# Kernel optimization log

Measured on AMD Instinct MI355X. Metric: run time of the kernel, lower is better.

The kernel has to match this reference:

```python
import jax, jax.numpy as jnp
import numpy as np

T, D, H, E, K = 8192, 2048, 7168, 8, 2


def setup_inputs() -> dict:
    key = jax.random.key(0)
    ks = jax.random.split(key, 5)
    s = 0.02
    return {
        "x": jax.random.normal(ks[0], (T, D), jnp.float32),
        "gate_w": jax.random.normal(ks[1], (E, D), jnp.float32) * s,
        "w1": jax.random.normal(ks[2], (E, H, D), jnp.float32) * s,
        "w2": jax.random.normal(ks[3], (E, H, D), jnp.float32) * s,
        "w3": jax.random.normal(ks[4], (E, H, D), jnp.float32) * s,
    }


def reference(x, gate_w, w1, w2, w3):
    # gate logits [T, E]
    logits = x @ gate_w.T
    vals, idx = jax.lax.top_k(logits, K)                      # [T, K]
    w = jax.nn.softmax(vals.astype(jnp.float32), axis=-1).astype(x.dtype)
    # per-token routing weight for each expert (0 if not selected) [T, E]
    tok = jnp.arange(x.shape[0])
    expert_w = jnp.zeros((x.shape[0], E), x.dtype).at[tok[:, None], idx].add(w)

    # scan over experts: dense SwiGLU per expert, weighted accumulate
    def body(acc, ws):
        w1e, w2e, w3e, we = ws  # [H,D],[H,D],[H,D],[T]
        y = (jax.nn.silu(x @ w1e.T) * (x @ w3e.T)) @ w2e      # [T, D]
        return acc + we[:, None] * y, None

    res, _ = jax.lax.scan(body, jnp.zeros_like(x), (w1, w2, w3, expert_w.T))
    return res
```

## Files before the change

### kernel.cpp

```cpp
#include <hip/hip_runtime.h>

#define TT   8192
#define DDIM 2048
#define HDIM 7168
#define NEXP 8
#define MT   32
#define NT1  (HDIM / 128)
#define NT2  (DDIM / 256)

typedef __attribute__((ext_vector_type(8))) short bf16x8;
typedef __attribute__((ext_vector_type(4))) short short4v;
typedef __attribute__((ext_vector_type(4))) float f32x4;

__device__ __forceinline__ unsigned short f2bf(float f) {
  unsigned int u = __builtin_bit_cast(unsigned int, f);
  u += 0x7fffu + ((u >> 16) & 1u);
  return (unsigned short)(u >> 16);
}

__device__ __forceinline__ void gload_lds16(const void* gp, void* lp) {
  __builtin_amdgcn_global_load_lds((__attribute__((address_space(1))) void*)gp,
                                   (__attribute__((address_space(3))) void*)lp,
                                   16, 0, 0);
}

__device__ __forceinline__ void mfma16(f32x4& c, bf16x8 a, bf16x8 b) {
  c = __builtin_amdgcn_mfma_f32_16x16x32_bf16(a, b, c, 0, 0, 0);
}

__device__ __forceinline__ void wg_barrier() {
  asm volatile("" ::: "memory");
  __builtin_amdgcn_s_barrier();
  asm volatile("" ::: "memory");
}

#define PH(H, BA, BB, RDB, STG, SRCP, SOFF, VM)                              \
  do {                                                                       \
    if (RDB) {                                                               \
      _Pragma("unroll")                                                      \
      for (int n = 0; n < 4; ++n)                                            \
        bfr[n] = *(const bf16x8*)(smem + (BB) + rB + n * 1024);              \
    }                                                                        \
    _Pragma("unroll")                                                        \
    for (int m = 0; m < 4; ++m)                                              \
      af[m] = *(const bf16x8*)(smem + (BA) + rA + ((H) + m) * 1024);         \
    if ((STG) >= 0) {                                                        \
      gload_lds16(SRCP[0] + (SOFF), smem + (STG) + wid * 2048);              \
      gload_lds16(SRCP[1] + (SOFF), smem + (STG) + wid * 2048 + 1024);       \
    }                                                                        \
    wg_barrier();                                                            \
    asm volatile("s_waitcnt lgkmcnt(0)" ::: "memory");                       \
    __builtin_amdgcn_sched_barrier(0);                                       \
    __builtin_amdgcn_s_setprio(1);                                           \
    _Pragma("unroll")                                                        \
    for (int n = 0; n < 4; ++n) {                                            \
      _Pragma("unroll")                                                      \
      for (int m = 0; m < 4; ++m)                                            \
        mfma16(acc[(H) + m][n], af[m], bfr[n]);                              \
    }                                                                        \
    __builtin_amdgcn_s_setprio(0);                                           \
    if ((VM) == 6) asm volatile("s_waitcnt vmcnt(6)" ::: "memory");          \
    if ((VM) == 0) asm volatile("s_waitcnt vmcnt(0)" ::: "memory");          \
    wg_barrier();                                                            \
  } while (0)

#define ITER_FULL(kb)                                                        \
  PH(0, 0,     32768,  1, 81920,  asrc, (kb) + 192, -1);                     \
  PH(4, 0,     32768,  0, 32768,  bsrc, (kb) + 256, -1);                     \
  PH(0, 16384, 49152,  1, 0,      asrc, (kb) + 256, -1);                     \
  PH(4, 16384, 49152,  0, 49152,  bsrc, (kb) + 320,  6);                     \
  PH(0, 65536, 98304,  1, 16384,  asrc, (kb) + 320, -1);                     \
  PH(4, 65536, 98304,  0, 98304,  bsrc, (kb) + 384, -1);                     \
  PH(0, 81920, 114688, 1, 65536,  asrc, (kb) + 384, -1);                     \
  PH(4, 81920, 114688, 0, 114688, bsrc, (kb) + 448,  6);

#define ITER_LAST(kb)                                                        \
  PH(0, 0,     32768,  1, 81920,  asrc, (kb) + 192, -1);                     \
  PH(4, 0,     32768,  0, -1,     asrc, 0,          -1);                     \
  PH(0, 16384, 49152,  1, -1,     asrc, 0,          -1);                     \
  PH(4, 16384, 49152,  0, -1,     asrc, 0,           0);                     \
  PH(0, 65536, 98304,  1, -1,     asrc, 0,          -1);                     \
  PH(4, 65536, 98304,  0, -1,     asrc, 0,          -1);                     \
  PH(0, 81920, 114688, 1, -1,     asrc, 0,          -1);                     \
  PH(4, 81920, 114688, 0, -1,     asrc, 0,          -1);

#define PROLOGUE()                                                           \
  do {                                                                       \
    gload_lds16(asrc[0] + 0,   smem + 0      + wid * 2048);                  \
    gload_lds16(asrc[1] + 0,   smem + 0      + wid * 2048 + 1024);           \
    gload_lds16(bsrc[0] + 0,   smem + 32768  + wid * 2048);                  \
    gload_lds16(bsrc[1] + 0,   smem + 32768  + wid * 2048 + 1024);           \
    gload_lds16(asrc[0] + 64,  smem + 16384  + wid * 2048);                  \
    gload_lds16(asrc[1] + 64,  smem + 16384  + wid * 2048 + 1024);           \
    gload_lds16(bsrc[0] + 64,  smem + 49152  + wid * 2048);                  \
    gload_lds16(bsrc[1] + 64,  smem + 49152  + wid * 2048 + 1024);           \
    gload_lds16(bsrc[0] + 128, smem + 98304  + wid * 2048);                  \
    gload_lds16(bsrc[1] + 128, smem + 98304  + wid * 2048 + 1024);           \
    gload_lds16(asrc[0] + 128, smem + 65536  + wid * 2048);                  \
    gload_lds16(asrc[1] + 128, smem + 65536  + wid * 2048 + 1024);           \
    gload_lds16(bsrc[0] + 192, smem + 114688 + wid * 2048);                  \
    gload_lds16(bsrc[1] + 192, smem + 114688 + wid * 2048 + 1024);           \
    asm volatile("s_waitcnt vmcnt(6)" ::: "memory");                         \
    wg_barrier();                                                            \
  } while (0)

__global__ __launch_bounds__(256) void cvt_bf16_kernel(const float* __restrict__ src,
                                                       unsigned short* __restrict__ dst,
                                                       long n4) {
  long i = (long)blockIdx.x * 256 + threadIdx.x;
  long stride = (long)gridDim.x * 256;
  for (; i < n4; i += stride) {
    float4 v = ((const float4*)src)[i];
    short4v s;
    s[0] = (short)f2bf(v.x); s[1] = (short)f2bf(v.y);
    s[2] = (short)f2bf(v.z); s[3] = (short)f2bf(v.w);
    ((short4v*)dst)[i] = s;
  }
}

__global__ __launch_bounds__(256) void gate_kernel(const float* __restrict__ x,
                                                   const float* __restrict__ gw,
                                                   int* __restrict__ route_e,
                                                   float* __restrict__ route_w,
                                                   int* __restrict__ counts) {
  int t = blockIdx.x;
  int tid = threadIdx.x;
  const float* xr = x + (size_t)t * DDIM;
  float p[NEXP];
#pragma unroll
  for (int e = 0; e < NEXP; ++e) p[e] = 0.f;
#pragma unroll
  for (int c = 0; c < DDIM / (256 * 4); ++c) {
    int d = (c * 256 + tid) * 4;
    float4 xv = *(const float4*)(xr + d);
#pragma unroll
    for (int e = 0; e < NEXP; ++e) {
      float4 wv = *(const float4*)(gw + (size_t)e * DDIM + d);
      p[e] += xv.x * wv.x + xv.y * wv.y + xv.z * wv.z + xv.w * wv.w;
    }
  }
  __shared__ float red[NEXP][4];
  int lane = tid & 63, wid = tid >> 6;
#pragma unroll
  for (int e = 0; e < NEXP; ++e) {
    float v = p[e];
    for (int o = 32; o > 0; o >>= 1) v += __shfl_down(v, o);
    if (lane == 0) red[e][wid] = v;
  }
  __syncthreads();
  if (tid == 0) {
    float lg[NEXP];
#pragma unroll
    for (int e = 0; e < NEXP; ++e) lg[e] = red[e][0] + red[e][1] + red[e][2] + red[e][3];
    int i0 = 0;
#pragma unroll
    for (int e = 1; e < NEXP; ++e) if (lg[e] > lg[i0]) i0 = e;
    int i1 = -1;
#pragma unroll
    for (int e = 0; e < NEXP; ++e) {
      if (e == i0) continue;
      if (i1 < 0 || lg[e] > lg[i1]) i1 = e;
    }
    float w0 = 1.f / (1.f + __expf(lg[i1] - lg[i0]));
    float w1 = 1.f - w0;
    route_e[t * 2 + 0] = i0;  route_e[t * 2 + 1] = i1;
    route_w[t * 2 + 0] = w0;  route_w[t * 2 + 1] = w1;
    atomicAdd(&counts[i0], 1);
    atomicAdd(&counts[i1], 1);
  }
}

__global__ void scan_kernel(const int* __restrict__ counts, int* __restrict__ offsets,
                            int* __restrict__ cursor) {
  if (threadIdx.x == 0 && blockIdx.x == 0) {
    int o = 0;
    for (int e = 0; e < NEXP; ++e) { offsets[e] = o; cursor[e] = o; o += counts[e]; }
  }
}

__global__ __launch_bounds__(256) void scatter_kernel(const int* __restrict__ route_e,
                                                      const float* __restrict__ route_w,
                                                      int* __restrict__ cursor,
                                                      int* __restrict__ tok_list,
                                                      float* __restrict__ tok_w) {
  int t = blockIdx.x * 256 + threadIdx.x;
  if (t >= TT) return;
#pragma unroll
  for (int s = 0; s < 2; ++s) {
    int e = route_e[t * 2 + s];
    int p = atomicAdd(&cursor[e], 1);
    tok_list[p] = t;
    tok_w[p] = route_w[t * 2 + s];
  }
}

__global__ __launch_bounds__(256) void transpose_w2_kernel(const float* __restrict__ w2,
                                                           unsigned short* __restrict__ w2t,
                                                           int expert_fixed) {
  int e = expert_fixed >= 0 ? expert_fixed : (int)blockIdx.z;
  const float* src = w2 + (size_t)e * HDIM * DDIM;
  unsigned short* dst = w2t + (expert_fixed >= 0 ? (size_t)0 : (size_t)e * DDIM * HDIM);
  int h0 = blockIdx.x * 64, d0 = blockIdx.y * 64;
  __shared__ __align__(8) unsigned short tile[64 * 66];
  int tid = threadIdx.x;
  int hr = tid >> 2;
#pragma unroll
  for (int j = 0; j < 4; ++j) {
    int f4 = (tid & 3) + j * 4;
    float4 v = *(const float4*)(src + (size_t)(h0 + hr) * DDIM + d0 + f4 * 4);
    unsigned int lo = (unsigned int)f2bf(v.x) | ((unsigned int)f2bf(v.y) << 16);
    unsigned int hi = (unsigned int)f2bf(v.z) | ((unsigned int)f2bf(v.w) << 16);
    char* bp = (char*)tile + hr * 132 + f4 * 8;
    *(unsigned int*)bp = lo;
    *(unsigned int*)(bp + 4) = hi;
  }
  __syncthreads();
  int dr = tid >> 2;
  int hbase = (tid & 3) * 16;
  unsigned short vals[16];
#pragma unroll
  for (int i = 0; i < 16; ++i)
    vals[i] = *(unsigned short*)((char*)tile + (hbase + i) * 132 + dr * 2);
  unsigned short* op = dst + (size_t)(d0 + dr) * HDIM + h0 + hbase;
#pragma unroll
  for (int j = 0; j < 4; ++j) {
    short4v s;
    s[0] = (short)vals[j * 4 + 0]; s[1] = (short)vals[j * 4 + 1];
    s[2] = (short)vals[j * 4 + 2]; s[3] = (short)vals[j * 4 + 3];
    *(short4v*)(op + j * 4) = s;
  }
}

__global__ __launch_bounds__(512, 2) void gemm1_kernel(
    const unsigned short* __restrict__ xbf, const unsigned short* __restrict__ w1b,
    const unsigned short* __restrict__ w3b, const int* __restrict__ tok_list,
    const int* __restrict__ counts, const int* __restrict__ offsets,
    unsigned short* __restrict__ g, int expert_fixed) {
  __shared__ __align__(16) char smem[133120];
  constexpr int NI = DDIM / 128;

  int nwg = gridDim.x;
  int orig = blockIdx.x;
  int wg = (orig & 7) * (nwg >> 3) + (orig >> 3);
  int mt = wg & (MT - 1);
  int rem = wg >> 5;
  int nt = rem % NT1;
  int e = expert_fixed >= 0 ? expert_fixed : rem / NT1;

  int cnt = counts[e];
  int mbase = mt * 256;
  if (mbase >= cnt) return;
  int off = offsets[e];
  int gshift = expert_fixed >= 0 ? 0 : off;
  int rows = cnt - mbase; if (rows > 256) rows = 256;

  const unsigned short* w1e = expert_fixed >= 0 ? w1b : w1b + (size_t)e * HDIM * DDIM;
  const unsigned short* w3e = expert_fixed >= 0 ? w3b : w3b + (size_t)e * HDIM * DDIM;

  int tid = threadIdx.x, lane = tid & 63, wid = tid >> 6;
  int wr = wid >> 2, wc = wid & 3;

  int r16 = lane >> 2;
  int csrc = (lane & 3) ^ ((lane >> 3) & 3);
  const char* asrc[2]; const char* bsrc[2];
#pragma unroll
  for (int j = 0; j < 2; ++j) {
    int r = wid * 32 + j * 16 + r16;
    int m = mbase + r; if (m > cnt - 1) m = cnt - 1;
    int tok = tok_list[off + m];
    asrc[j] = (const char*)xbf + (size_t)tok * (DDIM * 2) + csrc * 16;
    const char* base = (r < 128)
        ? (const char*)w1e + (size_t)(nt * 128 + r) * (DDIM * 2)
        : (const char*)w3e + (size_t)(nt * 128 + r - 128) * (DDIM * 2);
    bsrc[j] = base + csrc * 16;
  }
  int rA = (wr * 128 + (lane & 15)) * 64 + (((lane >> 4) ^ ((lane >> 1) & 3)) * 16);
  int rB = (wc * 64  + (lane & 15)) * 64 + (((lane >> 4) ^ ((lane >> 1) & 3)) * 16);

  f32x4 zv = {0.f, 0.f, 0.f, 0.f};
  f32x4 acc[8][4];
#pragma unroll
  for (int m = 0; m < 8; ++m)
#pragma unroll
    for (int n = 0; n < 4; ++n) acc[m][n] = zv;
  bf16x8 af[4], bfr[4];

  PROLOGUE();
#pragma unroll 1
  for (int i = 0; i < NI - 1; ++i) {
    size_t kb = (size_t)i * 256;
    ITER_FULL(kb);
  }
  {
    size_t kb = (size_t)(NI - 1) * 256;
    ITER_LAST(kb);
  }

  float* hb = (float*)smem;
  if (wc < 2) {
#pragma unroll
    for (int m = 0; m < 8; ++m)
#pragma unroll
      for (int q = 0; q < 4; ++q) {
        int row = wr * 128 + m * 16 + (lane >> 4) * 4 + q;
        int col = wc * 64 + (lane & 15);
#pragma unroll
        for (int n = 0; n < 4; ++n)
          hb[row * 130 + col + n * 16] = acc[m][n][q];
      }
  }
  asm volatile("s_waitcnt lgkmcnt(0)" ::: "memory");
  wg_barrier();
  if (wc >= 2) {
#pragma unroll
    for (int m = 0; m < 8; ++m)
#pragma unroll
      for (int q = 0; q < 4; ++q) {
        int row = wr * 128 + m * 16 + (lane >> 4) * 4 + q;
        if (row >= rows) continue;
        size_t grow = (size_t)(mbase + row + gshift);
        int colbase = (wc - 2) * 64 + (lane & 15);
        unsigned short* gp = g + grow * HDIM + nt * 128 + colbase;
#pragma unroll
        for (int n = 0; n < 4; ++n) {
          float h1 = hb[row * 130 + colbase + n * 16];
          float h3 = acc[m][n][q];
          float gv = (h1 / (1.f + __expf(-h1))) * h3;
          gp[n * 16] = f2bf(gv);
        }
      }
  }
}

__global__ __launch_bounds__(512, 2) void gemm2_kernel(
    const unsigned short* __restrict__ g, const unsigned short* __restrict__ w2t,
    const int* __restrict__ tok_list, const float* __restrict__ tok_w,
    const int* __restrict__ counts, const int* __restrict__ offsets,
    float* __restrict__ out, int expert_fixed) {
  __shared__ __align__(16) char smem[131072];
  constexpr int NI = HDIM / 128;

  int nwg = gridDim.x;
  int orig = blockIdx.x;
  int wg = (orig & 7) * (nwg >> 3) + (orig >> 3);
  int mt = wg & (MT - 1);
  int rem = wg >> 5;
  int nt = rem % NT2;
  int e = expert_fixed >= 0 ? expert_fixed : rem / NT2;

  int cnt = counts[e];
  int mbase = mt * 256;
  if (mbase >= cnt) return;
  int off = offsets[e];
  int gshift = expert_fixed >= 0 ? 0 : off;
  int nbase = nt * 256;
  int rows = cnt - mbase; if (rows > 256) rows = 256;
  const unsigned short* w2te = w2t + (expert_fixed >= 0 ? (size_t)0 : (size_t)e * DDIM * HDIM);

  int tid = threadIdx.x, lane = tid & 63, wid = tid >> 6;
  int wr = wid >> 2, wc = wid & 3;

  int r16 = lane >> 2;
  int csrc = (lane & 3) ^ ((lane >> 3) & 3);
  const char* asrc[2]; const char* bsrc[2];
#pragma unroll
  for (int j = 0; j < 2; ++j) {
    int r = wid * 32 + j * 16 + r16;
    int m = mbase + r; if (m > cnt - 1) m = cnt - 1;
    asrc[j] = (const char*)g + (size_t)(m + gshift) * (HDIM * 2) + csrc * 16;
    bsrc[j] = (const char*)w2te + (size_t)(nbase + r) * (HDIM * 2) + csrc * 16;
  }
  int rA = (wr * 128 + (lane & 15)) * 64 + (((lane >> 4) ^ ((lane >> 1) & 3)) * 16);
  int rB = (wc * 64  + (lane & 15)) * 64 + (((lane >> 4) ^ ((lane >> 1) & 3)) * 16);

  f32x4 zv = {0.f, 0.f, 0.f, 0.f};
  f32x4 acc[8][4];
#pragma unroll
  for (int m = 0; m < 8; ++m)
#pragma unroll
    for (int n = 0; n < 4; ++n) acc[m][n] = zv;
  bf16x8 af[4], bfr[4];

  PROLOGUE();
#pragma unroll 1
  for (int i = 0; i < NI - 1; ++i) {
    size_t kb = (size_t)i * 256;
    ITER_FULL(kb);
  }
  {
    size_t kb = (size_t)(NI - 1) * 256;
    ITER_LAST(kb);
  }

#pragma unroll
  for (int m = 0; m < 8; ++m)
#pragma unroll
    for (int q = 0; q < 4; ++q) {
      int row = wr * 128 + m * 16 + (lane >> 4) * 4 + q;
      if (row >= rows) continue;
      int mi = mbase + row;
      int tok = tok_list[off + mi];
      float wt = tok_w[off + mi];
      float* op = out + (size_t)tok * DDIM + nbase + wc * 64 + (lane & 15);
#pragma unroll
      for (int n = 0; n < 4; ++n)
        atomicAdd(op + n * 16, acc[m][n][q] * wt);
    }
}

extern "C" void kernel_launch(void* const* d_in, const int* in_sizes, int n_in,
                              void* d_out, int out_size, void* d_ws, size_t ws_size,
                              hipStream_t stream) {
  const float* x      = (const float*)d_in[0];
  const float* gate_w = (const float*)d_in[1];
  const float* w1     = (const float*)d_in[2];
  const float* w2     = (const float*)d_in[3];
  const float* w3     = (const float*)d_in[4];
  float* out = (float*)d_out;
  char* ws = (char*)d_ws;

  size_t o = 0;
  int* counts  = (int*)(ws + o);
  int* offsets = counts + 8;
  int* cursor  = counts + 16;
  o += 256;
  int*   route_e = (int*)(ws + o);   o += (size_t)TT * 2 * 4;
  float* route_w = (float*)(ws + o); o += (size_t)TT * 2 * 4;
  int*   tok_list = (int*)(ws + o);  o += (size_t)TT * 2 * 4;
  float* tok_w = (float*)(ws + o);   o += (size_t)TT * 2 * 4;
  unsigned short* xbf = (unsigned short*)(ws + o); o += (size_t)TT * DDIM * 2;
  size_t fixed = o;

  const size_t WSZ = (size_t)HDIM * DDIM;
  const size_t wbf_full = (size_t)NEXP * WSZ * 2;
  const size_t gfull = (size_t)TT * 2 * HDIM * 2;

  hipMemsetAsync(counts, 0, 8 * sizeof(int), stream);
  hipMemsetAsync(out, 0, (size_t)TT * DDIM * sizeof(float), stream);
  cvt_bf16_kernel<<<4096, 256, 0, stream>>>(x, xbf, (long)TT * DDIM / 4);
  gate_kernel<<<TT, 256, 0, stream>>>(x, gate_w, route_e, route_w, counts);
  scan_kernel<<<1, 64, 0, stream>>>(counts, offsets, cursor);
  scatter_kernel<<<(TT + 255) / 256, 256, 0, stream>>>(route_e, route_w, cursor, tok_list, tok_w);

  if (ws_size >= fixed + 3 * wbf_full + gfull) {
    unsigned short* w1b = (unsigned short*)(ws + fixed);
    unsigned short* w3b = w1b + NEXP * WSZ;
    unsigned short* w2t = w3b + NEXP * WSZ;
    unsigned short* gbuf = w2t + NEXP * WSZ;
    cvt_bf16_kernel<<<8192, 256, 0, stream>>>(w1, w1b, (long)(NEXP * WSZ / 4));
    cvt_bf16_kernel<<<8192, 256, 0, stream>>>(w3, w3b, (long)(NEXP * WSZ / 4));
    transpose_w2_kernel<<<dim3(HDIM / 64, DDIM / 64, NEXP), 256, 0, stream>>>(w2, w2t, -1);
    gemm1_kernel<<<MT * NT1 * NEXP, 512, 0, stream>>>(
        xbf, w1b, w3b, tok_list, counts, offsets, gbuf, -1);
    gemm2_kernel<<<MT * NT2 * NEXP, 512, 0, stream>>>(
        gbuf, w2t, tok_list, tok_w, counts, offsets, out, -1);
  } else {
    unsigned short* w1b = (unsigned short*)(ws + fixed);
    unsigned short* w3b = w1b + WSZ;
    unsigned short* w2t = w3b + WSZ;
    unsigned short* gbuf = w2t + WSZ;
    for (int e = 0; e < NEXP; ++e) {
      cvt_bf16_kernel<<<4096, 256, 0, stream>>>(w1 + (size_t)e * WSZ, w1b, (long)(WSZ / 4));
      cvt_bf16_kernel<<<4096, 256, 0, stream>>>(w3 + (size_t)e * WSZ, w3b, (long)(WSZ / 4));
      transpose_w2_kernel<<<dim3(HDIM / 64, DDIM / 64, 1), 256, 0, stream>>>(w2, w2t, e);
      gemm1_kernel<<<MT * NT1, 512, 0, stream>>>(
          xbf, w1b, w3b, tok_list, counts, offsets, gbuf, e);
      gemm2_kernel<<<MT * NT2, 512, 0, stream>>>(
          gbuf, w2t, tok_list, tok_w, counts, offsets, out, e);
    }
  }
}
```

Measured before the change: 2.491 ms.

## Double-buffer LDS fragment reads to overlap ds_read with MFMA in GEMM phases

Each phase now issues the LDS reads for the next phase's A/B fragments into alternate register buffers (af0/af1, bf0/bf1) before running the current phase's MFMAs. The lgkmcnt waits are partial, so only the data needed now must have arrived. The reads use inline-asm ds_read_b128, and the vmcnt waits are retuned. The aim is to hide LDS read latency behind matrix math, at the cost of more vector registers, which could affect occupancy or cause spills.

```diff
diff --git a/kernel.cpp b/kernel.cpp
--- a/kernel.cpp
+++ b/kernel.cpp
@@ -11,6 +11,7 @@
 typedef __attribute__((ext_vector_type(8))) short bf16x8;
 typedef __attribute__((ext_vector_type(4))) short short4v;
 typedef __attribute__((ext_vector_type(4))) float f32x4;
+typedef const __attribute__((address_space(3))) char* lds_ptr;
 
 __device__ __forceinline__ unsigned short f2bf(float f) {
   unsigned int u = __builtin_bit_cast(unsigned int, f);
@@ -28,61 +29,72 @@
   c = __builtin_amdgcn_mfma_f32_16x16x32_bf16(a, b, c, 0, 0, 0);
 }
 
+__device__ __forceinline__ bf16x8 ds_read128(lds_ptr p) {
+  bf16x8 r;
+  asm volatile("ds_read_b128 %0, %1" : "=&v"(r) : "v"(p));
+  return r;
+}
+
 __device__ __forceinline__ void wg_barrier() {
   asm volatile("" ::: "memory");
   __builtin_amdgcn_s_barrier();
   asm volatile("" ::: "memory");
 }
 
-#define PH(H, BA, BB, RDB, STG, SRCP, SOFF, VM)                              \
+#define PH2(HH, AF, BF, NBA, AFN, NBB, BFN, STG, SRCP, SOFF, LGK, VM)        \
   do {                                                                       \
-    if (RDB) {                                                               \
+    if ((NBA) >= 0) {                                                        \
+      _Pragma("unroll")                                                      \
+      for (int m = 0; m < 4; ++m)                                            \
+        AFN[m] = ds_read128(lds3 + (NBA) + rA + m * 1024);                   \
+    }                                                                        \
+    if ((NBB) >= 0) {                                                        \
       _Pragma("unroll")                                                      \
       for (int n = 0; n < 4; ++n)                                            \
-        bfr[n] = *(const bf16x8*)(smem + (BB) + rB + n * 1024);              \
+        BFN[n] = ds_read128(lds3 + (NBB) + rB + n * 1024);                   \
     }                                                                        \
-    _Pragma("unroll")                                                        \
-    for (int m = 0; m < 4; ++m)                                              \
-      af[m] = *(const bf16x8*)(smem + (BA) + rA + ((H) + m) * 1024);         \
     if ((STG) >= 0) {                                                        \
       gload_lds16(SRCP[0] + (SOFF), smem + (STG) + wid * 2048);              \
       gload_lds16(SRCP[1] + (SOFF), smem + (STG) + wid * 2048 + 1024);       \
     }                                                                        \
     wg_barrier();                                                            \
-    asm volatile("s_waitcnt lgkmcnt(0)" ::: "memory");                       \
+    if ((LGK) == 8) asm volatile("s_waitcnt lgkmcnt(8)" ::: "memory");       \
+    if ((LGK) == 4) asm volatile("s_waitcnt lgkmcnt(4)" ::: "memory");       \
+    if ((LGK) == 0) asm volatile("s_waitcnt lgkmcnt(0)" ::: "memory");       \
     __builtin_amdgcn_sched_barrier(0);                                       \
     __builtin_amdgcn_s_setprio(1);                                           \
     _Pragma("unroll")                                                        \
     for (int n = 0; n < 4; ++n) {                                            \
       _Pragma("unroll")                                                      \
       for (int m = 0; m < 4; ++m)                                            \
-        mfma16(acc[(H) + m][n], af[m], bfr[n]);                              \
+        mfma16(acc[(HH) + m][n], AF[m], BF[n]);                              \
     }                                                                        \
     __builtin_amdgcn_s_setprio(0);                                           \
-    if ((VM) == 6) asm volatile("s_waitcnt vmcnt(6)" ::: "memory");          \
+    __builtin_amdgcn_sched_barrier(0);                                       \
+    if ((VM) == 8) asm volatile("s_waitcnt vmcnt(8)" ::: "memory");          \
     if ((VM) == 0) asm volatile("s_waitcnt vmcnt(0)" ::: "memory");          \
     wg_barrier();                                                            \
   } while (0)
 
-#define ITER_FULL(kb)                                                        \
-  PH(0, 0,     32768,  1, 81920,  asrc, (kb) + 192, -1);                     \
-  PH(4, 0,     32768,  0, 32768,  bsrc, (kb) + 256, -1);                     \
-  PH(0, 16384, 49152,  1, 0,      asrc, (kb) + 256, -1);                     \
-  PH(4, 16384, 49152,  0, 49152,  bsrc, (kb) + 320,  6);                     \
-  PH(0, 65536, 98304,  1, 16384,  asrc, (kb) + 320, -1);                     \
-  PH(4, 65536, 98304,  0, 98304,  bsrc, (kb) + 384, -1);                     \
-  PH(0, 81920, 114688, 1, 65536,  asrc, (kb) + 384, -1);                     \
-  PH(4, 81920, 114688, 0, 114688, bsrc, (kb) + 448,  6);
-
-#define ITER_LAST(kb)                                                        \
-  PH(0, 0,     32768,  1, 81920,  asrc, (kb) + 192, -1);                     \
-  PH(4, 0,     32768,  0, -1,     asrc, 0,          -1);                     \
-  PH(0, 16384, 49152,  1, -1,     asrc, 0,          -1);                     \
-  PH(4, 16384, 49152,  0, -1,     asrc, 0,           0);                     \
-  PH(0, 65536, 98304,  1, -1,     asrc, 0,          -1);                     \
-  PH(4, 65536, 98304,  0, -1,     asrc, 0,          -1);                     \
-  PH(0, 81920, 114688, 1, -1,     asrc, 0,          -1);                     \
-  PH(4, 81920, 114688, 0, -1,     asrc, 0,          -1);
+#define ITER_FULL2(kb)                                                         \
+  PH2(0, af1, bf0, 4096,  af0, -1,     bf1, 81920,  asrc, (kb) + 192, 4, 8);   \
+  PH2(4, af0, bf0, 16384, af1, 49152,  bf1, 32768,  bsrc, (kb) + 256, 8, 8);   \
+  PH2(0, af1, bf1, 20480, af0, -1,     bf0, 0,      asrc, (kb) + 256, 4, 8);   \
+  PH2(4, af0, bf1, 65536, af1, 98304,  bf0, 49152,  bsrc, (kb) + 320, 8, 8);   \
+  PH2(0, af1, bf0, 69632, af0, -1,     bf1, 16384,  asrc, (kb) + 320, 4, 8);   \
+  PH2(4, af0, bf0, 81920, af1, 114688, bf1, 98304,  bsrc, (kb) + 384, 8, 8);   \
+  PH2(0, af1, bf1, 86016, af0, -1,     bf0, 65536,  asrc, (kb) + 384, 4, 8);   \
+  PH2(4, af0, bf1, 0,     af1, 32768,  bf0, 114688, bsrc, (kb) + 448, 8, 8);
+
+#define ITER_LAST2(kb)                                                         \
+  PH2(0, af1, bf0, 4096,  af0, -1,     bf1, 81920, asrc, (kb) + 192, 4, 8);    \
+  PH2(4, af0, bf0, 16384, af1, 49152,  bf1, -1,    asrc, 0,          8, 8);    \
+  PH2(0, af1, bf1, 20480, af0, -1,     bf0, -1,    asrc, 0,          4, 8);    \
+  PH2(4, af0, bf1, 65536, af1, 98304,  bf0, -1,    asrc, 0,          8, 0);    \
+  PH2(0, af1, bf0, 69632, af0, -1,     bf1, -1,    asrc, 0,          4, 8);    \
+  PH2(4, af0, bf0, 81920, af1, 114688, bf1, -1,    asrc, 0,          8, 8);    \
+  PH2(0, af1, bf1, 86016, af0, -1,     bf0, -1,    asrc, 0,          4, 8);    \
+  PH2(4, af0, bf1, -1,    af1, -1,     bf0, -1,    asrc, 0,          0, 8);
 
 #define PROLOGUE()                                                           \
   do {                                                                       \
@@ -102,6 +114,12 @@
     gload_lds16(bsrc[1] + 192, smem + 114688 + wid * 2048 + 1024);           \
     asm volatile("s_waitcnt vmcnt(6)" ::: "memory");                         \
     wg_barrier();                                                            \
+    _Pragma("unroll")                                                        \
+    for (int m = 0; m < 4; ++m)                                              \
+      af1[m] = ds_read128(lds3 + 0 + rA + m * 1024);                         \
+    _Pragma("unroll")                                                        \
+    for (int n = 0; n < 4; ++n)                                              \
+      bf0[n] = ds_read128(lds3 + 32768 + rB + n * 1024);                     \
   } while (0)
 
 __global__ __launch_bounds__(256) void cvt_bf16_kernel(const float* __restrict__ src,
@@ -259,6 +277,7 @@
 
   int tid = threadIdx.x, lane = tid & 63, wid = tid >> 6;
   int wr = wid >> 2, wc = wid & 3;
+  lds_ptr lds3 = (lds_ptr)smem;
 
   int r16 = lane >> 2;
   int csrc = (lane & 3) ^ ((lane >> 3) & 3);
@@ -283,17 +302,17 @@
   for (int m = 0; m < 8; ++m)
 #pragma unroll
     for (int n = 0; n < 4; ++n) acc[m][n] = zv;
-  bf16x8 af[4], bfr[4];
+  bf16x8 af0[4], af1[4], bf0[4], bf1[4];
 
   PROLOGUE();
 #pragma unroll 1
   for (int i = 0; i < NI - 1; ++i) {
     size_t kb = (size_t)i * 256;
-    ITER_FULL(kb);
+    ITER_FULL2(kb);
   }
   {
     size_t kb = (size_t)(NI - 1) * 256;
-    ITER_LAST(kb);
+    ITER_LAST2(kb);
   }
 
   float* hb = (float*)smem;
@@ -359,6 +378,7 @@
 
   int tid = threadIdx.x, lane = tid & 63, wid = tid >> 6;
   int wr = wid >> 2, wc = wid & 3;
+  lds_ptr lds3 = (lds_ptr)smem;
 
   int r16 = lane >> 2;
   int csrc = (lane & 3) ^ ((lane >> 3) & 3);
@@ -379,17 +399,17 @@
   for (int m = 0; m < 8; ++m)
 #pragma unroll
     for (int n = 0; n < 4; ++n) acc[m][n] = zv;
-  bf16x8 af[4], bfr[4];
+  bf16x8 af0[4], af1[4], bf0[4], bf1[4];
 
   PROLOGUE();
 #pragma unroll 1
   for (int i = 0; i < NI - 1; ++i) {
     size_t kb = (size_t)i * 256;
-    ITER_FULL(kb);
+    ITER_FULL2(kb);
   }
   {
     size_t kb = (size_t)(NI - 1) * 256;
-    ITER_LAST(kb);
+    ITER_LAST2(kb);
   }
 
 #pragma unroll
```

Result: slower. 3.156 ms (+26.7%).

## Merge half-phases into full 8x4 MFMA phases with joint A/B staging

Applied to the files above, without the earlier changes.

Restructures the software-pipelined GEMM main loop from eight half-tile phases per iteration into four full phases. Each phase now loads all 8 A fragments and 4 B fragments, issues 32 MFMAs, and stages both the A and B tiles for a later k-block at once. The prologue and vmcnt waits are adjusted to match. This halves the number of workgroup barriers per iteration and gives larger MFMA bursts, at the cost of more live VGPRs for fragments and a shallower prefetch lead for the B tiles.

```diff
diff --git a/kernel.cpp b/kernel.cpp
--- a/kernel.cpp
+++ b/kernel.cpp
@@ -34,19 +34,21 @@
   asm volatile("" ::: "memory");
 }
 
-#define PH(H, BA, BB, RDB, STG, SRCP, SOFF, VM)                              \
+#define PH4(BA, BB, SA, AO, SB, BO, VM)                                      \
   do {                                                                       \
-    if (RDB) {                                                               \
-      _Pragma("unroll")                                                      \
-      for (int n = 0; n < 4; ++n)                                            \
-        bfr[n] = *(const bf16x8*)(smem + (BB) + rB + n * 1024);              \
+    _Pragma("unroll")                                                        \
+    for (int m = 0; m < 8; ++m)                                              \
+      af[m] = *(const bf16x8*)(smem + (BA) + rA + m * 1024);                 \
+    _Pragma("unroll")                                                        \
+    for (int n = 0; n < 4; ++n)                                              \
+      bfr[n] = *(const bf16x8*)(smem + (BB) + rB + n * 1024);                \
+    if ((SA) >= 0) {                                                         \
+      gload_lds16(asrc[0] + (AO), smem + (SA) + wid * 2048);                 \
+      gload_lds16(asrc[1] + (AO), smem + (SA) + wid * 2048 + 1024);          \
     }                                                                        \
-    _Pragma("unroll")                                                        \
-    for (int m = 0; m < 4; ++m)                                              \
-      af[m] = *(const bf16x8*)(smem + (BA) + rA + ((H) + m) * 1024);         \
-    if ((STG) >= 0) {                                                        \
-      gload_lds16(SRCP[0] + (SOFF), smem + (STG) + wid * 2048);              \
-      gload_lds16(SRCP[1] + (SOFF), smem + (STG) + wid * 2048 + 1024);       \
+    if ((SB) >= 0) {                                                         \
+      gload_lds16(bsrc[0] + (BO), smem + (SB) + wid * 2048);                 \
+      gload_lds16(bsrc[1] + (BO), smem + (SB) + wid * 2048 + 1024);          \
     }                                                                        \
     wg_barrier();                                                            \
     asm volatile("s_waitcnt lgkmcnt(0)" ::: "memory");                       \
@@ -55,34 +57,28 @@
     _Pragma("unroll")                                                        \
     for (int n = 0; n < 4; ++n) {                                            \
       _Pragma("unroll")                                                      \
-      for (int m = 0; m < 4; ++m)                                            \
-        mfma16(acc[(H) + m][n], af[m], bfr[n]);                              \
+      for (int m = 0; m < 8; ++m)                                            \
+        mfma16(acc[m][n], af[m], bfr[n]);                                    \
     }                                                                        \
     __builtin_amdgcn_s_setprio(0);                                           \
-    if ((VM) == 6) asm volatile("s_waitcnt vmcnt(6)" ::: "memory");          \
+    __builtin_amdgcn_sched_barrier(0);                                       \
+    if ((VM) == 8) asm volatile("s_waitcnt vmcnt(8)" ::: "memory");          \
+    if ((VM) == 4) asm volatile("s_waitcnt vmcnt(4)" ::: "memory");          \
     if ((VM) == 0) asm volatile("s_waitcnt vmcnt(0)" ::: "memory");          \
     wg_barrier();                                                            \
   } while (0)
 
-#define ITER_FULL(kb)                                                        \
-  PH(0, 0,     32768,  1, 81920,  asrc, (kb) + 192, -1);                     \
-  PH(4, 0,     32768,  0, 32768,  bsrc, (kb) + 256, -1);                     \
-  PH(0, 16384, 49152,  1, 0,      asrc, (kb) + 256, -1);                     \
-  PH(4, 16384, 49152,  0, 49152,  bsrc, (kb) + 320,  6);                     \
-  PH(0, 65536, 98304,  1, 16384,  asrc, (kb) + 320, -1);                     \
-  PH(4, 65536, 98304,  0, 98304,  bsrc, (kb) + 384, -1);                     \
-  PH(0, 81920, 114688, 1, 65536,  asrc, (kb) + 384, -1);                     \
-  PH(4, 81920, 114688, 0, 114688, bsrc, (kb) + 448,  6);
-
-#define ITER_LAST(kb)                                                        \
-  PH(0, 0,     32768,  1, 81920,  asrc, (kb) + 192, -1);                     \
-  PH(4, 0,     32768,  0, -1,     asrc, 0,          -1);                     \
-  PH(0, 16384, 49152,  1, -1,     asrc, 0,          -1);                     \
-  PH(4, 16384, 49152,  0, -1,     asrc, 0,           0);                     \
-  PH(0, 65536, 98304,  1, -1,     asrc, 0,          -1);                     \
-  PH(4, 65536, 98304,  0, -1,     asrc, 0,          -1);                     \
-  PH(0, 81920, 114688, 1, -1,     asrc, 0,          -1);                     \
-  PH(4, 81920, 114688, 0, -1,     asrc, 0,          -1);
+#define ITER4_FULL(kb)                                                       \
+  PH4(0,     32768,  81920, (kb) + 192, 114688, (kb) + 192, 8);              \
+  PH4(16384, 49152,  0,     (kb) + 256, 32768,  (kb) + 256, 8);              \
+  PH4(65536, 98304,  16384, (kb) + 320, 49152,  (kb) + 320, 8);              \
+  PH4(81920, 114688, 65536, (kb) + 384, 98304,  (kb) + 384, 8);
+
+#define ITER4_LAST(kb)                                                       \
+  PH4(0,     32768,  81920, (kb) + 192, 114688, (kb) + 192, 8);              \
+  PH4(16384, 49152,  -1,    0,          -1,     0,          4);              \
+  PH4(65536, 98304,  -1,    0,          -1,     0,          0);              \
+  PH4(81920, 114688, -1,    0,          -1,     0,          -1);
 
 #define PROLOGUE()                                                           \
   do {                                                                       \
@@ -94,13 +90,11 @@
     gload_lds16(asrc[1] + 64,  smem + 16384  + wid * 2048 + 1024);           \
     gload_lds16(bsrc[0] + 64,  smem + 49152  + wid * 2048);                  \
     gload_lds16(bsrc[1] + 64,  smem + 49152  + wid * 2048 + 1024);           \
+    gload_lds16(asrc[0] + 128, smem + 65536  + wid * 2048);                  \
+    gload_lds16(asrc[1] + 128, smem + 65536  + wid * 2048 + 1024);           \
     gload_lds16(bsrc[0] + 128, smem + 98304  + wid * 2048);                  \
     gload_lds16(bsrc[1] + 128, smem + 98304  + wid * 2048 + 1024);           \
-    gload_lds16(asrc[0] + 128, smem + 65536  + wid * 2048);                  \
-    gload_lds16(asrc[1] + 128, smem + 65536  + wid * 2048 + 1024);           \
-    gload_lds16(bsrc[0] + 192, smem + 114688 + wid * 2048);                  \
-    gload_lds16(bsrc[1] + 192, smem + 114688 + wid * 2048 + 1024);           \
-    asm volatile("s_waitcnt vmcnt(6)" ::: "memory");                         \
+    asm volatile("s_waitcnt vmcnt(8)" ::: "memory");                         \
     wg_barrier();                                                            \
   } while (0)
 
@@ -283,17 +277,17 @@
   for (int m = 0; m < 8; ++m)
 #pragma unroll
     for (int n = 0; n < 4; ++n) acc[m][n] = zv;
-  bf16x8 af[4], bfr[4];
+  bf16x8 af[8], bfr[4];
 
   PROLOGUE();
 #pragma unroll 1
   for (int i = 0; i < NI - 1; ++i) {
     size_t kb = (size_t)i * 256;
-    ITER_FULL(kb);
+    ITER4_FULL(kb);
   }
   {
     size_t kb = (size_t)(NI - 1) * 256;
-    ITER_LAST(kb);
+    ITER4_LAST(kb);
   }
 
   float* hb = (float*)smem;
@@ -379,17 +373,17 @@
   for (int m = 0; m < 8; ++m)
 #pragma unroll
     for (int n = 0; n < 4; ++n) acc[m][n] = zv;
-  bf16x8 af[4], bfr[4];
+  bf16x8 af[8], bfr[4];
 
   PROLOGUE();
 #pragma unroll 1
   for (int i = 0; i < NI - 1; ++i) {
     size_t kb = (size_t)i * 256;
-    ITER_FULL(kb);
+    ITER4_FULL(kb);
   }
   {
     size_t kb = (size_t)(NI - 1) * 256;
-    ITER_LAST(kb);
+    ITER4_LAST(kb);
   }
 
 #pragma unroll
```

Result: slower. 2.720 ms (+9.2%).
